# Kernel optimization log

Measured on AMD Instinct MI355X. Metric: run time of the kernel, lower is better.

Reference implementation:

```python
import jax, jax.numpy as jnp
import numpy as np

N = 100000   # number of website nodes
E = 800000   # edges per edge type
F = 128      # in_feats == out_feats
NEG_SLOPE = 0.2


def setup_inputs() -> dict:
    key = jax.random.key(0)
    ks = jax.random.split(key, 16)
    s = 1.0 / np.sqrt(F)
    return {
        "feat": jax.random.normal(ks[0], (N, F), jnp.float32),
        "src_u": jax.random.randint(ks[1], (E,), 0, N),
        "dst_u": jax.random.randint(ks[2], (E,), 0, N),
        "src_r": jax.random.randint(ks[3], (E,), 0, N),
        "dst_r": jax.random.randint(ks[4], (E,), 0, N),
        # fc_self (no bias)
        "W_self": jax.random.uniform(ks[5], (F, F), jnp.float32, -s, s),
        # attn branch 'user'
        "W_u": jax.random.uniform(ks[6], (F, F), jnp.float32, -s, s),
        "a_l_u": jax.random.uniform(ks[7], (F,), jnp.float32, -s, s),
        "a_r_u": jax.random.uniform(ks[8], (F,), jnp.float32, -s, s),
        # attn branch 'reuse'
        "W_r": jax.random.uniform(ks[9], (F, F), jnp.float32, -s, s),
        "a_l_r": jax.random.uniform(ks[10], (F,), jnp.float32, -s, s),
        "a_r_r": jax.random.uniform(ks[11], (F,), jnp.float32, -s, s),
        # fc_neigh (with bias)
        "W_neigh": jax.random.uniform(ks[12], (F, F), jnp.float32, -s, s),
        "b_neigh": jax.random.uniform(ks[13], (F,), jnp.float32, -s, s),
        # module-level bias parameter
        "bias": jnp.zeros((F,), jnp.float32),
    }


def _attn_aggregate(feat, W, a_l, a_r, src, dst, n_nodes):
    """GAT-style single-head aggregation over one edge type.
    Returns [n_nodes, F] = sum_{e: dst(e)=v} softmax_v(leaky_relu(el[src]+er[dst])) * h[src]."""
    h = feat @ W                                    # [N, F] (feat_src == feat_dst)
    el = h @ a_l                                    # [N]
    er = h @ a_r                                    # [N]
    e = jax.nn.leaky_relu(el[src] + er[dst], NEG_SLOPE)   # [E]
    # edge_softmax: normalize over incoming edges of each dst node
    m = jax.ops.segment_max(e, dst, num_segments=n_nodes)  # [N] (-inf for isolated dst, unused)
    ex = jnp.exp(e - m[dst])                        # [E]
    denom = jax.ops.segment_sum(ex, dst, num_segments=n_nodes)  # [N]
    a = ex / denom[dst]                             # [E]
    msg = h[src] * a[:, None]                       # [E, F]
    return jax.ops.segment_sum(msg, dst, num_segments=n_nodes)  # [N, F]


def reference(feat, src_u, dst_u, src_r, dst_r, W_self, W_u, a_l_u, a_r_u,
              W_r, a_l_r, a_r_r, W_neigh, b_neigh, bias):
    n = feat.shape[0]
    neigh_u = _attn_aggregate(feat, W_u, a_l_u, a_r_u, src_u, dst_u, n)
    neigh_r = _attn_aggregate(feat, W_r, a_l_r, a_r_r, src_r, dst_r, n)
    # multi_update_all cross reducer 'mean' over the two edge types
    neigh = 0.5 * (neigh_u + neigh_r)
    h_neigh = neigh @ W_neigh + b_neigh             # fc_neigh
    rst = feat @ W_self + h_neigh                   # fc_self(h_self) + h_neigh
    return rst + bias
```

## Files before the change

### kernel.cpp

```cpp
#include <hip/hip_runtime.h>

#define F 128
#define NEG_SLOPE 0.2f
#define SHIFT 9
#define BPB 512
#define NBS 512

typedef _Float16 f16_t;
typedef _Float16 f16x8 __attribute__((ext_vector_type(8)));
typedef _Float16 f16x2 __attribute__((ext_vector_type(2)));
typedef float f32x4 __attribute__((ext_vector_type(4)));

__global__ __launch_bounds__(128) void prep_mats(
    const float* __restrict__ Wu, const float* __restrict__ Wr,
    const float* __restrict__ Ws, const float* __restrict__ Wn,
    const float* __restrict__ alu, const float* __restrict__ aru,
    const float* __restrict__ alr, const float* __restrict__ arr_,
    f16_t* __restrict__ Mtu, f16_t* __restrict__ Mtr, f16_t* __restrict__ Wts,
    float* __restrict__ wlu, float* __restrict__ wru,
    float* __restrict__ wlr, float* __restrict__ wrr)
{
    int b = blockIdx.x;
    int tid = threadIdx.x;
    if (b < 256) {
        int k = b & 127;
        const float* W = (b < 128) ? Wu : Wr;
        f16_t* M = (b < 128) ? Mtu : Mtr;
        float acc = 0.f;
        for (int t = 0; t < F; t++) acc += W[k * F + t] * Wn[t * F + tid];
        M[tid * F + k] = (f16_t)acc;
    } else if (b < 384) {
        int c = b - 256;
        Wts[c * F + tid] = (f16_t)Ws[tid * F + c];
    } else {
        int which = b - 384;
        const float* W = (which < 2) ? Wu : Wr;
        const float* a = (which == 0) ? alu : (which == 1) ? aru : (which == 2) ? alr : arr_;
        float acc = 0.f;
        for (int c = 0; c < F; c++) acc += W[tid * F + c] * a[c];
        float* o = (which == 0) ? wlu : (which == 1) ? wru : (which == 2) ? wlr : wrr;
        o[tid] = acc;
    }
}


__global__ __launch_bounds__(256) void cast_p1a(
    const float* __restrict__ feat,
    const float* __restrict__ wlu, const float* __restrict__ wru,
    const float* __restrict__ wlr, const float* __restrict__ wrr,
    f16_t* __restrict__ featb,
    float* __restrict__ elu, float* __restrict__ eru,
    float* __restrict__ elr, float* __restrict__ err_,
    const int* __restrict__ dst_u, const int* __restrict__ dst_r,
    int* __restrict__ cnt_bb,
    int Eu, int Et, int N, int chunk, int n, int nbk)
{
    int b = blockIdx.x;
    int tid = threadIdx.x;
    if (b < 256) {
        __shared__ int hist[NBS];
        for (int i = tid; i < NBS; i += 256) hist[i] = 0;
        __syncthreads();
        int e0 = b * chunk;
        int e1 = e0 + chunk; if (e1 > Et) e1 = Et;
        int u1 = (e1 < Eu) ? e1 : Eu;
        for (int e = e0 + tid; e < u1; e += 256) {
            int bin = dst_u[e];
            atomicAdd(&hist[bin >> SHIFT], 1);
        }
        int r0 = (e0 > Eu) ? e0 : Eu;
        for (int e = r0 + tid; e < e1; e += 256) {
            int bin = N + dst_r[e - Eu];
            atomicAdd(&hist[bin >> SHIFT], 1);
        }
        __syncthreads();
        for (int i = tid; i < NBS; i += 256) cnt_bb[b * NBS + i] = hist[i];
        return;
    }
    int fid = b - 256;
    int lane = tid & 63;
    int wave = tid >> 6;
    int lo = lane & 15, hi = lane >> 4;
    int base = fid * 64 + wave * 16;
    if (base >= n) return;
    int row = base + lo;
    if (row > n - 1) row = n - 1;
    const float* fp = feat + (size_t)row * F + hi * 8;
    f16_t* fb = featb + (size_t)row * F + hi * 8;
    const float* wsel = (lo == 0) ? wlu : (lo == 1) ? wru : (lo == 2) ? wlr : wrr;

    f32x4 acc = (f32x4){0.f, 0.f, 0.f, 0.f};
#pragma unroll
    for (int ks = 0; ks < 4; ks++) {
        float4 a0 = *(const float4*)(fp + ks * 32);
        float4 a1 = *(const float4*)(fp + ks * 32 + 4);
        f16x8 af;
        af[0] = (f16_t)a0.x; af[1] = (f16_t)a0.y; af[2] = (f16_t)a0.z; af[3] = (f16_t)a0.w;
        af[4] = (f16_t)a1.x; af[5] = (f16_t)a1.y; af[6] = (f16_t)a1.z; af[7] = (f16_t)a1.w;
        *(f16x8*)(fb + ks * 32) = af;
        f16x8 bf;
#pragma unroll
        for (int q = 0; q < 8; q++) bf[q] = (f16_t)0;
        if (lo < 4) {
            float4 b0 = *(const float4*)(wsel + ks * 32 + hi * 8);
            float4 b1 = *(const float4*)(wsel + ks * 32 + hi * 8 + 4);
            bf[0] = (f16_t)b0.x; bf[1] = (f16_t)b0.y; bf[2] = (f16_t)b0.z; bf[3] = (f16_t)b0.w;
            bf[4] = (f16_t)b1.x; bf[5] = (f16_t)b1.y; bf[6] = (f16_t)b1.z; bf[7] = (f16_t)b1.w;
        }
        acc = __builtin_amdgcn_mfma_f32_16x16x32_f16(af, bf, acc, 0, 0, 0);
    }
    if (lo < 4) {
        float* oarr = (lo == 0) ? elu : (lo == 1) ? eru : (lo == 2) ? elr : err_;
#pragma unroll
        for (int j = 0; j < 4; j++) {
            int r = base + hi * 4 + j;
            if (r < n) oarr[r] = acc[j];
        }
    }
}


__global__ __launch_bounds__(256) void scan_bb1(int* __restrict__ cnt_bb,
                                                int* __restrict__ btot, int nbk)
{
    int k = blockIdx.x;
    int tid = threadIdx.x;
    __shared__ int lds[256];
    int v = cnt_bb[tid * NBS + k];
    lds[tid] = v;
    __syncthreads();
    for (int off = 1; off < 256; off <<= 1) {
        int add = (tid >= off) ? lds[tid - off] : 0;
        __syncthreads();
        lds[tid] += add;
        __syncthreads();
    }
    cnt_bb[tid * NBS + k] = lds[tid] - v;
    if (tid == 255) btot[k] = lds[255];
}


__global__ __launch_bounds__(512) void scan_bb2(const int* __restrict__ btot,
                                                int* __restrict__ bbase,
                                                int* __restrict__ rp,
                                                int nbk, int twoN, int Et)
{
    __shared__ int lds[512];
    int t = threadIdx.x;
    int v = (t < nbk) ? btot[t] : 0;
    lds[t] = v;
    __syncthreads();
    for (int off = 1; off < 512; off <<= 1) {
        int add = (t >= off) ? lds[t - off] : 0;
        __syncthreads();
        lds[t] += add;
        __syncthreads();
    }
    bbase[t] = lds[t] - v;
    if (t == 0) rp[twoN] = Et;
}


__global__ __launch_bounds__(256) void p1b_scatter(
    const int* __restrict__ src_u, const int* __restrict__ dst_u,
    const int* __restrict__ src_r, const int* __restrict__ dst_r,
    const int* __restrict__ cnt_bb, const int* __restrict__ bbase,
    uint2* __restrict__ bucketed,
    int Eu, int Et, int N, int chunk, int nbk)
{
    int b = blockIdx.x;
    int tid = threadIdx.x;
    __shared__ int cur[NBS];
    for (int i = tid; i < nbk; i += 256) cur[i] = bbase[i] + cnt_bb[b * NBS + i];
    __syncthreads();
    int e0 = b * chunk;
    int e1 = e0 + chunk; if (e1 > Et) e1 = Et;
    int u1 = (e1 < Eu) ? e1 : Eu;
    for (int e = e0 + tid; e < u1; e += 256) {
        int bin = dst_u[e];
        int s = src_u[e];
        int pos = atomicAdd(&cur[bin >> SHIFT], 1);
        bucketed[pos] = make_uint2((unsigned)s, (unsigned)bin);
    }
    int r0 = (e0 > Eu) ? e0 : Eu;
    for (int e = r0 + tid; e < e1; e += 256) {
        int bin = N + dst_r[e - Eu];
        int s = src_r[e - Eu];
        int pos = atomicAdd(&cur[bin >> SHIFT], 1);
        bucketed[pos] = make_uint2((unsigned)s, (unsigned)bin);
    }
}


__global__ __launch_bounds__(256) void p2_build(
    const uint2* __restrict__ bucketed, const int* __restrict__ bbase,
    int* __restrict__ rp, int* __restrict__ csr, int twoN)
{
    int k = blockIdx.x;
    int tid = threadIdx.x;
    int beg = bbase[k], end = bbase[k + 1];
    __shared__ int hist[BPB];
    __shared__ int psum[256];
    for (int i = tid; i < BPB; i += 256) hist[i] = 0;
    __syncthreads();
    for (int i = beg + tid; i < end; i += 256) {
        uint2 p = bucketed[i];
        atomicAdd(&hist[p.y & (BPB - 1)], 1);
    }
    __syncthreads();
    int a0 = hist[2 * tid], a1 = hist[2 * tid + 1];
    psum[tid] = a0 + a1;
    __syncthreads();
    for (int off = 1; off < 256; off <<= 1) {
        int add = (tid >= off) ? psum[tid - off] : 0;
        __syncthreads();
        psum[tid] += add;
        __syncthreads();
    }
    int base0 = beg + psum[tid] - (a0 + a1);
    int bin0 = (k << SHIFT) + 2 * tid;
    if (bin0 < twoN)     rp[bin0]     = base0;
    if (bin0 + 1 < twoN) rp[bin0 + 1] = base0 + a0;
    __syncthreads();
    hist[2 * tid]     = base0;
    hist[2 * tid + 1] = base0 + a0;
    __syncthreads();
    for (int i = beg + tid; i < end; i += 256) {
        uint2 p = bucketed[i];
        int pos = atomicAdd(&hist[p.y & (BPB - 1)], 1);
        csr[pos] = (int)p.x;
    }
}


__global__ __launch_bounds__(256) void aggregate_fused(
    const f16_t* __restrict__ featb,
    const float* __restrict__ elu, const float* __restrict__ eru,
    const float* __restrict__ elr, const float* __restrict__ err_,
    const int* __restrict__ rp, const int* __restrict__ csr,
    f16_t* __restrict__ aggu, f16_t* __restrict__ aggr, int n)
{
    int wid = (int)(((size_t)blockIdx.x * 256 + threadIdx.x) >> 6);
    if (wid >= n) return;
    int lane = threadIdx.x & 63;
    int g = lane >> 4, lo = lane & 15;

    int begu = rp[wid],     endu = rp[wid + 1];
    int begr = rp[n + wid], endr = rp[n + wid + 1];
    float ervu = eru[wid];
    float ervr = err_[wid];

    union UP { f16x2 h; int i; };
    union UV { f16x8 v; f16x2 p[4]; };

    f16x2 z = {(f16_t)0, (f16_t)0};
    f16x2 au0 = z, au1 = z, au2 = z, au3 = z;
    f16x2 ar0 = z, ar1 = z, ar2 = z, ar3 = z;
    float du = 0.f, dr = 0.f;

    int iu = begu + g, ir = begr + g;
    int su = (iu < endu) ? csr[iu] : 0;
    int sr = (ir < endr) ? csr[ir] : 0;

    while (iu < endu || ir < endr) {
        int su2 = (iu + 4 < endu) ? csr[iu + 4] : 0;
        int sr2 = (ir + 4 < endr) ? csr[ir + 4] : 0;
        if (iu < endu) {
            float e = elu[su] + ervu;
            e = fmaxf(e, NEG_SLOPE * e);
            float ex = __expf(e);
            f16_t exh = (f16_t)ex;
            f16x2 exv = {exh, exh};
            UV hc; hc.v = *(const f16x8*)&featb[(size_t)su * F + lo * 8];
            au0 += exv * hc.p[0];
            au1 += exv * hc.p[1];
            au2 += exv * hc.p[2];
            au3 += exv * hc.p[3];
            du += ex;
        }
        if (ir < endr) {
            float e = elr[sr] + ervr;
            e = fmaxf(e, NEG_SLOPE * e);
            float ex = __expf(e);
            f16_t exh = (f16_t)ex;
            f16x2 exv = {exh, exh};
            UV hc; hc.v = *(const f16x8*)&featb[(size_t)sr * F + lo * 8];
            ar0 += exv * hc.p[0];
            ar1 += exv * hc.p[1];
            ar2 += exv * hc.p[2];
            ar3 += exv * hc.p[3];
            dr += ex;
        }
        iu += 4; ir += 4; su = su2; sr = sr2;
    }

#pragma unroll
    for (int off = 16; off < 64; off <<= 1) {
        du += __shfl_xor(du, off);
        dr += __shfl_xor(dr, off);
        UP x;
        x.h = au0; x.i = __shfl_xor(x.i, off); au0 += x.h;
        x.h = au1; x.i = __shfl_xor(x.i, off); au1 += x.h;
        x.h = au2; x.i = __shfl_xor(x.i, off); au2 += x.h;
        x.h = au3; x.i = __shfl_xor(x.i, off); au3 += x.h;
        x.h = ar0; x.i = __shfl_xor(x.i, off); ar0 += x.h;
        x.h = ar1; x.i = __shfl_xor(x.i, off); ar1 += x.h;
        x.h = ar2; x.i = __shfl_xor(x.i, off); ar2 += x.h;
        x.h = ar3; x.i = __shfl_xor(x.i, off); ar3 += x.h;
    }

    if (g == 0) {
        float invu = (du > 0.f) ? 0.5f / du : 0.f;
        float invr = (dr > 0.f) ? 0.5f / dr : 0.f;
        f16_t ihu = (f16_t)invu, ihr = (f16_t)invr;
        f16x2 ivu = {ihu, ihu}, ivr = {ihr, ihr};
        UV ou, orr;
        ou.p[0] = au0 * ivu; ou.p[1] = au1 * ivu; ou.p[2] = au2 * ivu; ou.p[3] = au3 * ivu;
        orr.p[0] = ar0 * ivr; orr.p[1] = ar1 * ivr; orr.p[2] = ar2 * ivr; orr.p[3] = ar3 * ivr;
        *(f16x8*)&aggu[(size_t)wid * F + lo * 8] = ou.v;
        *(f16x8*)&aggr[(size_t)wid * F + lo * 8] = orr.v;
    }
}


__global__ __launch_bounds__(1024) void mfma_final3(
    const f16_t* __restrict__ featb,
    const f16_t* __restrict__ aggu, const f16_t* __restrict__ aggr,
    const f16_t* __restrict__ Wts, const f16_t* __restrict__ Mtu,
    const f16_t* __restrict__ Mtr,
    const float* __restrict__ bn, const float* __restrict__ bias,
    float* __restrict__ out, int n, int ntiles)
{
    __shared__ f16_t Ls[F * F];
    __shared__ f16_t Lu[F * F];
    __shared__ f16_t Lr[F * F];
    for (int i = threadIdx.x; i < 2048; i += 1024) {
        int c = i >> 4, kc = i & 15, kcs = kc ^ (c & 15);
        *(f16x8*)&Ls[c * F + kcs * 8] = *(const f16x8*)&Wts[c * F + kc * 8];
        *(f16x8*)&Lu[c * F + kcs * 8] = *(const f16x8*)&Mtu[c * F + kc * 8];
        *(f16x8*)&Lr[c * F + kcs * 8] = *(const f16x8*)&Mtr[c * F + kc * 8];
    }
    __syncthreads();

    int lane = threadIdx.x & 63;
    int wave = threadIdx.x >> 6;
    int lo = lane & 15, hi = lane >> 4;

    float cb[8];
#pragma unroll
    for (int t = 0; t < 8; t++) cb[t] = bn[t * 16 + lo] + bias[t * 16 + lo];

    for (int tile = blockIdx.x; tile < ntiles; tile += 256) {
        int row0 = tile * 256 + wave * 16;
        if (row0 >= n) continue;
        int arow = row0 + lo;
        if (arow > n - 1) arow = n - 1;
        const f16_t* pf = featb + (size_t)arow * F + hi * 8;
        const f16_t* pu = aggu + (size_t)arow * F + hi * 8;
        const f16_t* pr = aggr + (size_t)arow * F + hi * 8;

        f32x4 acc[8];
#pragma unroll
        for (int t = 0; t < 8; t++) acc[t] = (f32x4){0.f, 0.f, 0.f, 0.f};

#pragma unroll
        for (int ks = 0; ks < 4; ks++) {
            f16x8 a1 = *(const f16x8*)(pf + ks * 32);
            f16x8 a2 = *(const f16x8*)(pu + ks * 32);
            f16x8 a3 = *(const f16x8*)(pr + ks * 32);
#pragma unroll
            for (int t = 0; t < 8; t++) {
                int c = t * 16 + lo;
                int kcs = (ks * 4 + hi) ^ lo;
                f16x8 bs = *(const f16x8*)&Ls[c * F + kcs * 8];
                f16x8 bu = *(const f16x8*)&Lu[c * F + kcs * 8];
                f16x8 br = *(const f16x8*)&Lr[c * F + kcs * 8];
                acc[t] = __builtin_amdgcn_mfma_f32_16x16x32_f16(a1, bs, acc[t], 0, 0, 0);
                acc[t] = __builtin_amdgcn_mfma_f32_16x16x32_f16(a2, bu, acc[t], 0, 0, 0);
                acc[t] = __builtin_amdgcn_mfma_f32_16x16x32_f16(a3, br, acc[t], 0, 0, 0);
            }
        }

#pragma unroll
        for (int j = 0; j < 4; j++) {
            int r = row0 + hi * 4 + j;
            if (r < n) {
                float* op = out + (size_t)r * F + lo;
#pragma unroll
                for (int t = 0; t < 8; t++) op[t * 16] = acc[t][j] + cb[t];
            }
        }
    }
}


extern "C" void kernel_launch(void* const* d_in, const int* in_sizes, int n_in,
                              void* d_out, int out_size, void* d_ws, size_t ws_size,
                              hipStream_t stream) {
    const float* feat   = (const float*)d_in[0];
    const int*   src_u  = (const int*)d_in[1];
    const int*   dst_u  = (const int*)d_in[2];
    const int*   src_r  = (const int*)d_in[3];
    const int*   dst_r  = (const int*)d_in[4];
    const float* W_self = (const float*)d_in[5];
    const float* W_u    = (const float*)d_in[6];
    const float* a_l_u  = (const float*)d_in[7];
    const float* a_r_u  = (const float*)d_in[8];
    const float* W_r    = (const float*)d_in[9];
    const float* a_l_r  = (const float*)d_in[10];
    const float* a_r_r  = (const float*)d_in[11];
    const float* W_ngh  = (const float*)d_in[12];
    const float* b_ngh  = (const float*)d_in[13];
    const float* bias   = (const float*)d_in[14];
    float* out = (float*)d_out;

    const int N  = in_sizes[0] / F;
    const int Eu = in_sizes[1];
    const int Er = in_sizes[3];
    const int Et = Eu + Er;
    const int twoN = 2 * N;
    const int nbk = (twoN + BPB - 1) >> SHIFT;

    char* ws = (char*)d_ws;
    size_t off = 0;
    auto alloc = [&](size_t bytes) -> void* {
        void* p = ws + off;
        off = (off + bytes + 255) & ~(size_t)255;
        return p;
    };
    f16_t* featb = (f16_t*)alloc((size_t)N * F * 2);
    f16_t* aggu  = (f16_t*)alloc((size_t)N * F * 2);
    f16_t* aggr  = (f16_t*)alloc((size_t)N * F * 2);
    f16_t* Mt_u  = (f16_t*)alloc((size_t)F * F * 2);
    f16_t* Mt_r  = (f16_t*)alloc((size_t)F * F * 2);
    f16_t* Wt_s  = (f16_t*)alloc((size_t)F * F * 2);
    float* wlu = (float*)alloc((size_t)F * 4);
    float* wru = (float*)alloc((size_t)F * 4);
    float* wlr = (float*)alloc((size_t)F * 4);
    float* wrr = (float*)alloc((size_t)F * 4);
    float* elu = (float*)alloc((size_t)N * 4);
    float* eru = (float*)alloc((size_t)N * 4);
    float* elr = (float*)alloc((size_t)N * 4);
    float* err_ = (float*)alloc((size_t)N * 4);
    int* cnt_bb = (int*)alloc((size_t)256 * NBS * 4);
    int* btot   = (int*)alloc((size_t)NBS * 4);
    int* bbase  = (int*)alloc((size_t)(NBS + 1) * 4);
    int* rp2    = (int*)alloc(((size_t)twoN + 1) * 4);
    uint2* bucketed = (uint2*)alloc((size_t)Et * 8);
    int* csr2   = (int*)alloc((size_t)Et * 4);

    prep_mats<<<388, 128, 0, stream>>>(W_u, W_r, W_self, W_ngh,
                                       a_l_u, a_r_u, a_l_r, a_r_r,
                                       Mt_u, Mt_r, Wt_s, wlu, wru, wlr, wrr);

    const int chunk = (Et + 255) / 256;
    int castBlocks = (N + 63) / 64;
    cast_p1a<<<256 + castBlocks, 256, 0, stream>>>(
        feat, wlu, wru, wlr, wrr, featb, elu, eru, elr, err_,
        dst_u, dst_r, cnt_bb, Eu, Et, N, chunk, N, nbk);

    scan_bb1<<<nbk, 256, 0, stream>>>(cnt_bb, btot, nbk);
    scan_bb2<<<1, 512, 0, stream>>>(btot, bbase, rp2, nbk, twoN, Et);
    p1b_scatter<<<256, 256, 0, stream>>>(src_u, dst_u, src_r, dst_r,
                                         cnt_bb, bbase, bucketed,
                                         Eu, Et, N, chunk, nbk);
    p2_build<<<nbk, 256, 0, stream>>>(bucketed, bbase, rp2, csr2, twoN);

    aggregate_fused<<<(N + 3) / 4, 256, 0, stream>>>(featb, elu, eru, elr, err_,
                                                     rp2, csr2, aggu, aggr, N);
    int ntiles = (N + 255) / 256;
    mfma_final3<<<256, 1024, 0, stream>>>(featb, aggu, aggr,
                                          Wt_s, Mt_u, Mt_r,
                                          b_ngh, bias, out, N, ntiles);
}
```

Before: 156.3 us.

## Precompute edge weights during CSR build and map 16-lane groups per destination

Packs each bucketed edge into one 32-bit word (17-bit source plus the bin's low bits), halving the bucket buffer traffic. The CSR build now also computes the leaky-relu exp attention weight per edge and stores it as fp16 next to the CSR, so aggregation no longer gathers el/er. The aggregation kernel gives each 16-lane group its own destination node instead of a whole wave, which removes the cross-group shuffle reduction, and it double-buffers two edges per type. This adds an fp16 edge-weight array and depends on node ids fitting in 17 bits. It also gives less parallelism per high-degree node.

```diff
diff --git a/kernel.cpp b/kernel.cpp
--- a/kernel.cpp
+++ b/kernel.cpp
@@ -139,7 +139,6 @@
     if (tid == 255) btot[k] = lds[255];
 }
 
-
 __global__ __launch_bounds__(512) void scan_bb2(const int* __restrict__ btot,
                                                 int* __restrict__ bbase,
                                                 int* __restrict__ rp,
@@ -165,7 +164,7 @@
     const int* __restrict__ src_u, const int* __restrict__ dst_u,
     const int* __restrict__ src_r, const int* __restrict__ dst_r,
     const int* __restrict__ cnt_bb, const int* __restrict__ bbase,
-    uint2* __restrict__ bucketed,
+    unsigned* __restrict__ bucketed,
     int Eu, int Et, int N, int chunk, int nbk)
 {
     int b = blockIdx.x;
@@ -180,21 +179,24 @@
         int bin = dst_u[e];
         int s = src_u[e];
         int pos = atomicAdd(&cur[bin >> SHIFT], 1);
-        bucketed[pos] = make_uint2((unsigned)s, (unsigned)bin);
+        bucketed[pos] = (unsigned)s | ((unsigned)(bin & (BPB - 1)) << 17);
     }
     int r0 = (e0 > Eu) ? e0 : Eu;
     for (int e = r0 + tid; e < e1; e += 256) {
         int bin = N + dst_r[e - Eu];
         int s = src_r[e - Eu];
         int pos = atomicAdd(&cur[bin >> SHIFT], 1);
-        bucketed[pos] = make_uint2((unsigned)s, (unsigned)bin);
+        bucketed[pos] = (unsigned)s | ((unsigned)(bin & (BPB - 1)) << 17);
     }
 }
 
 
 __global__ __launch_bounds__(256) void p2_build(
-    const uint2* __restrict__ bucketed, const int* __restrict__ bbase,
-    int* __restrict__ rp, int* __restrict__ csr, int twoN)
+    const unsigned* __restrict__ bucketed, const int* __restrict__ bbase,
+    const float* __restrict__ elu, const float* __restrict__ eru,
+    const float* __restrict__ elr, const float* __restrict__ err_,
+    int* __restrict__ rp, int* __restrict__ csr, f16_t* __restrict__ exh,
+    int twoN, int N)
 {
     int k = blockIdx.x;
     int tid = threadIdx.x;
@@ -204,8 +206,8 @@
     for (int i = tid; i < BPB; i += 256) hist[i] = 0;
     __syncthreads();
     for (int i = beg + tid; i < end; i += 256) {
-        uint2 p = bucketed[i];
-        atomicAdd(&hist[p.y & (BPB - 1)], 1);
+        unsigned w = bucketed[i];
+        atomicAdd(&hist[(w >> 17) & (BPB - 1)], 1);
     }
     __syncthreads();
     int a0 = hist[2 * tid], a1 = hist[2 * tid + 1];
@@ -226,90 +228,111 @@
     hist[2 * tid + 1] = base0 + a0;
     __syncthreads();
     for (int i = beg + tid; i < end; i += 256) {
-        uint2 p = bucketed[i];
-        int pos = atomicAdd(&hist[p.y & (BPB - 1)], 1);
-        csr[pos] = (int)p.x;
-    }
-}
-
-
-__global__ __launch_bounds__(256) void aggregate_fused(
-    const f16_t* __restrict__ featb,
-    const float* __restrict__ elu, const float* __restrict__ eru,
-    const float* __restrict__ elr, const float* __restrict__ err_,
+        unsigned w = bucketed[i];
+        int src = (int)(w & 0x1FFFF);
+        int binlow = (int)((w >> 17) & (BPB - 1));
+        int bin = (k << SHIFT) | binlow;
+        bool isu = bin < N;
+        const float* el = isu ? elu : elr;
+        const float* er = isu ? eru : err_;
+        int d = isu ? bin : bin - N;
+        float e = el[src] + er[d];
+        e = fmaxf(e, NEG_SLOPE * e);
+        float ex = __expf(e);
+        int pos = atomicAdd(&hist[binlow], 1);
+        csr[pos] = src;
+        exh[pos] = (f16_t)ex;
+    }
+}
+
+
+__global__ __launch_bounds__(256) void aggregate_v2(
+    const f16_t* __restrict__ featb, const f16_t* __restrict__ exh,
     const int* __restrict__ rp, const int* __restrict__ csr,
     f16_t* __restrict__ aggu, f16_t* __restrict__ aggr, int n)
 {
-    int wid = (int)(((size_t)blockIdx.x * 256 + threadIdx.x) >> 6);
-    if (wid >= n) return;
+    int wave = (int)(((size_t)blockIdx.x * 256 + threadIdx.x) >> 6);
     int lane = threadIdx.x & 63;
     int g = lane >> 4, lo = lane & 15;
-
-    int begu = rp[wid],     endu = rp[wid + 1];
-    int begr = rp[n + wid], endr = rp[n + wid + 1];
-    float ervu = eru[wid];
-    float ervr = err_[wid];
-
-    union UP { f16x2 h; int i; };
+    int dst = wave * 4 + g;
+    bool alive = (dst < n);
+    int dc = alive ? dst : (n - 1);
+
+    int begu = rp[dc], endu = rp[dc + 1];
+    int begr = rp[n + dc], endr = rp[n + dc + 1];
+    if (!alive) { endu = begu; endr = begr; }
+
     union UV { f16x8 v; f16x2 p[4]; };
-
     f16x2 z = {(f16_t)0, (f16_t)0};
     f16x2 au0 = z, au1 = z, au2 = z, au3 = z;
     f16x2 ar0 = z, ar1 = z, ar2 = z, ar3 = z;
     float du = 0.f, dr = 0.f;
 
-    int iu = begu + g, ir = begr + g;
-    int su = (iu < endu) ? csr[iu] : 0;
-    int sr = (ir < endr) ? csr[ir] : 0;
+    int iu = begu, ir = begr;
+
+    int a0 = (iu     < endu) ? iu     : 0;
+    int a1 = (iu + 1 < endu) ? iu + 1 : 0;
+    int b0 = (ir     < endr) ? ir     : 0;
+    int b1 = (ir + 1 < endr) ? ir + 1 : 0;
+    int cu0 = csr[a0], cu1 = csr[a1], cr0 = csr[b0], cr1 = csr[b1];
+    f16_t wu0 = (iu     < endu) ? exh[a0] : (f16_t)0;
+    f16_t wu1 = (iu + 1 < endu) ? exh[a1] : (f16_t)0;
+    f16_t wr0 = (ir     < endr) ? exh[b0] : (f16_t)0;
+    f16_t wr1 = (ir + 1 < endr) ? exh[b1] : (f16_t)0;
+    UV hu0, hu1, hr0, hr1;
+    hu0.v = *(const f16x8*)&featb[(size_t)cu0 * F + lo * 8];
+    hu1.v = *(const f16x8*)&featb[(size_t)cu1 * F + lo * 8];
+    hr0.v = *(const f16x8*)&featb[(size_t)cr0 * F + lo * 8];
+    hr1.v = *(const f16x8*)&featb[(size_t)cr1 * F + lo * 8];
 
     while (iu < endu || ir < endr) {
-        int su2 = (iu + 4 < endu) ? csr[iu + 4] : 0;
-        int sr2 = (ir + 4 < endr) ? csr[ir + 4] : 0;
-        if (iu < endu) {
-            float e = elu[su] + ervu;
-            e = fmaxf(e, NEG_SLOPE * e);
-            float ex = __expf(e);
-            f16_t exh = (f16_t)ex;
-            f16x2 exv = {exh, exh};
-            UV hc; hc.v = *(const f16x8*)&featb[(size_t)su * F + lo * 8];
-            au0 += exv * hc.p[0];
-            au1 += exv * hc.p[1];
-            au2 += exv * hc.p[2];
-            au3 += exv * hc.p[3];
-            du += ex;
-        }
-        if (ir < endr) {
-            float e = elr[sr] + ervr;
-            e = fmaxf(e, NEG_SLOPE * e);
-            float ex = __expf(e);
-            f16_t exh = (f16_t)ex;
-            f16x2 exv = {exh, exh};
-            UV hc; hc.v = *(const f16x8*)&featb[(size_t)sr * F + lo * 8];
-            ar0 += exv * hc.p[0];
-            ar1 += exv * hc.p[1];
-            ar2 += exv * hc.p[2];
-            ar3 += exv * hc.p[3];
-            dr += ex;
-        }
-        iu += 4; ir += 4; su = su2; sr = sr2;
-    }
-
-#pragma unroll
-    for (int off = 16; off < 64; off <<= 1) {
-        du += __shfl_xor(du, off);
-        dr += __shfl_xor(dr, off);
-        UP x;
-        x.h = au0; x.i = __shfl_xor(x.i, off); au0 += x.h;
-        x.h = au1; x.i = __shfl_xor(x.i, off); au1 += x.h;
-        x.h = au2; x.i = __shfl_xor(x.i, off); au2 += x.h;
-        x.h = au3; x.i = __shfl_xor(x.i, off); au3 += x.h;
-        x.h = ar0; x.i = __shfl_xor(x.i, off); ar0 += x.h;
-        x.h = ar1; x.i = __shfl_xor(x.i, off); ar1 += x.h;
-        x.h = ar2; x.i = __shfl_xor(x.i, off); ar2 += x.h;
-        x.h = ar3; x.i = __shfl_xor(x.i, off); ar3 += x.h;
-    }
-
-    if (g == 0) {
+        int ju = iu + 2, jr = ir + 2;
+        int na0 = (ju     < endu) ? ju     : 0;
+        int na1 = (ju + 1 < endu) ? ju + 1 : 0;
+        int nb0 = (jr     < endr) ? jr     : 0;
+        int nb1 = (jr + 1 < endr) ? jr + 1 : 0;
+        int ncu0 = csr[na0], ncu1 = csr[na1], ncr0 = csr[nb0], ncr1 = csr[nb1];
+        f16_t nwu0 = (ju     < endu) ? exh[na0] : (f16_t)0;
+        f16_t nwu1 = (ju + 1 < endu) ? exh[na1] : (f16_t)0;
+        f16_t nwr0 = (jr     < endr) ? exh[nb0] : (f16_t)0;
+        f16_t nwr1 = (jr + 1 < endr) ? exh[nb1] : (f16_t)0;
+        UV pu0, pu1, pr0, pr1;
+        pu0.v = *(const f16x8*)&featb[(size_t)ncu0 * F + lo * 8];
+        pu1.v = *(const f16x8*)&featb[(size_t)ncu1 * F + lo * 8];
+        pr0.v = *(const f16x8*)&featb[(size_t)ncr0 * F + lo * 8];
+        pr1.v = *(const f16x8*)&featb[(size_t)ncr1 * F + lo * 8];
+
+        {
+            f16x2 wv = {wu0, wu0};
+            au0 += wv * hu0.p[0]; au1 += wv * hu0.p[1];
+            au2 += wv * hu0.p[2]; au3 += wv * hu0.p[3];
+            du += (float)wu0;
+        }
+        {
+            f16x2 wv = {wu1, wu1};
+            au0 += wv * hu1.p[0]; au1 += wv * hu1.p[1];
+            au2 += wv * hu1.p[2]; au3 += wv * hu1.p[3];
+            du += (float)wu1;
+        }
+        {
+            f16x2 wv = {wr0, wr0};
+            ar0 += wv * hr0.p[0]; ar1 += wv * hr0.p[1];
+            ar2 += wv * hr0.p[2]; ar3 += wv * hr0.p[3];
+            dr += (float)wr0;
+        }
+        {
+            f16x2 wv = {wr1, wr1};
+            ar0 += wv * hr1.p[0]; ar1 += wv * hr1.p[1];
+            ar2 += wv * hr1.p[2]; ar3 += wv * hr1.p[3];
+            dr += (float)wr1;
+        }
+
+        hu0 = pu0; hu1 = pu1; hr0 = pr0; hr1 = pr1;
+        wu0 = nwu0; wu1 = nwu1; wr0 = nwr0; wr1 = nwr1;
+        iu = ju; ir = jr;
+    }
+
+    if (alive) {
         float invu = (du > 0.f) ? 0.5f / du : 0.f;
         float invr = (dr > 0.f) ? 0.5f / dr : 0.f;
         f16_t ihu = (f16_t)invu, ihr = (f16_t)invr;
@@ -317,8 +340,8 @@
         UV ou, orr;
         ou.p[0] = au0 * ivu; ou.p[1] = au1 * ivu; ou.p[2] = au2 * ivu; ou.p[3] = au3 * ivu;
         orr.p[0] = ar0 * ivr; orr.p[1] = ar1 * ivr; orr.p[2] = ar2 * ivr; orr.p[3] = ar3 * ivr;
-        *(f16x8*)&aggu[(size_t)wid * F + lo * 8] = ou.v;
-        *(f16x8*)&aggr[(size_t)wid * F + lo * 8] = orr.v;
+        *(f16x8*)&aggu[(size_t)dst * F + lo * 8] = ou.v;
+        *(f16x8*)&aggr[(size_t)dst * F + lo * 8] = orr.v;
     }
 }
 
@@ -446,8 +469,9 @@
     int* btot   = (int*)alloc((size_t)NBS * 4);
     int* bbase  = (int*)alloc((size_t)(NBS + 1) * 4);
     int* rp2    = (int*)alloc(((size_t)twoN + 1) * 4);
-    uint2* bucketed = (uint2*)alloc((size_t)Et * 8);
+    unsigned* bucketed = (unsigned*)alloc((size_t)Et * 4);
     int* csr2   = (int*)alloc((size_t)Et * 4);
+    f16_t* exh  = (f16_t*)alloc((size_t)Et * 2);
 
     prep_mats<<<388, 128, 0, stream>>>(W_u, W_r, W_self, W_ngh,
                                        a_l_u, a_r_u, a_l_r, a_r_r,
@@ -464,10 +488,11 @@
     p1b_scatter<<<256, 256, 0, stream>>>(src_u, dst_u, src_r, dst_r,
                                          cnt_bb, bbase, bucketed,
                                          Eu, Et, N, chunk, nbk);
-    p2_build<<<nbk, 256, 0, stream>>>(bucketed, bbase, rp2, csr2, twoN);
-
-    aggregate_fused<<<(N + 3) / 4, 256, 0, stream>>>(featb, elu, eru, elr, err_,
-                                                     rp2, csr2, aggu, aggr, N);
+    p2_build<<<nbk, 256, 0, stream>>>(bucketed, bbase, elu, eru, elr, err_,
+                                      rp2, csr2, exh, twoN, N);
+
+    aggregate_v2<<<(N + 15) / 16, 256, 0, stream>>>(featb, exh, rp2, csr2,
+                                                    aggu, aggr, N);
     int ntiles = (N + 255) / 256;
     mfma_final3<<<256, 1024, 0, stream>>>(featb, aggu, aggr,
                                           Wt_s, Mt_u, Mt_r,
```

After: 158.4 us. No clear change (+1.4%).

## Fuse attention aggregation into MFMA output kernel and pack bucketed edges to 32 bits

Applied to the files above, without the earlier changes.

The gather-aggregate kernel is merged into the MFMA projection kernel. Each lane now accumulates the softmax-weighted neighbour sum for one destination row directly in registers and feeds it to the MFMA as the A operand, so the f16 aggu/aggr intermediate buffers are no longer written and read back. Bucketed edges are packed into one 32-bit word (17-bit source plus 9-bit local bin) instead of a uint2, and p2_build now uses 512 threads with one bin per thread. The trade-off is that each lane walks a whole destination's edge list serially, so load balance is worse and register pressure in the fused kernel rises. The 17-bit packing also assumes N is below 131072.

```diff
diff --git a/kernel.cpp b/kernel.cpp
--- a/kernel.cpp
+++ b/kernel.cpp
@@ -139,7 +139,6 @@
     if (tid == 255) btot[k] = lds[255];
 }
 
-
 __global__ __launch_bounds__(512) void scan_bb2(const int* __restrict__ btot,
                                                 int* __restrict__ bbase,
                                                 int* __restrict__ rp,
@@ -165,7 +164,7 @@
     const int* __restrict__ src_u, const int* __restrict__ dst_u,
     const int* __restrict__ src_r, const int* __restrict__ dst_r,
     const int* __restrict__ cnt_bb, const int* __restrict__ bbase,
-    uint2* __restrict__ bucketed,
+    unsigned* __restrict__ bucketed,
     int Eu, int Et, int N, int chunk, int nbk)
 {
     int b = blockIdx.x;
@@ -180,152 +179,62 @@
         int bin = dst_u[e];
         int s = src_u[e];
         int pos = atomicAdd(&cur[bin >> SHIFT], 1);
-        bucketed[pos] = make_uint2((unsigned)s, (unsigned)bin);
+        bucketed[pos] = (unsigned)s | ((unsigned)(bin & (BPB - 1)) << 17);
     }
     int r0 = (e0 > Eu) ? e0 : Eu;
     for (int e = r0 + tid; e < e1; e += 256) {
         int bin = N + dst_r[e - Eu];
         int s = src_r[e - Eu];
         int pos = atomicAdd(&cur[bin >> SHIFT], 1);
-        bucketed[pos] = make_uint2((unsigned)s, (unsigned)bin);
-    }
-}
-
-
-__global__ __launch_bounds__(256) void p2_build(
-    const uint2* __restrict__ bucketed, const int* __restrict__ bbase,
+        bucketed[pos] = (unsigned)s | ((unsigned)(bin & (BPB - 1)) << 17);
+    }
+}
+
+
+__global__ __launch_bounds__(512) void p2_build(
+    const unsigned* __restrict__ bucketed, const int* __restrict__ bbase,
     int* __restrict__ rp, int* __restrict__ csr, int twoN)
 {
     int k = blockIdx.x;
     int tid = threadIdx.x;
     int beg = bbase[k], end = bbase[k + 1];
     __shared__ int hist[BPB];
-    __shared__ int psum[256];
-    for (int i = tid; i < BPB; i += 256) hist[i] = 0;
-    __syncthreads();
-    for (int i = beg + tid; i < end; i += 256) {
-        uint2 p = bucketed[i];
-        atomicAdd(&hist[p.y & (BPB - 1)], 1);
-    }
-    __syncthreads();
-    int a0 = hist[2 * tid], a1 = hist[2 * tid + 1];
-    psum[tid] = a0 + a1;
-    __syncthreads();
-    for (int off = 1; off < 256; off <<= 1) {
+    __shared__ int psum[512];
+    hist[tid] = 0;
+    __syncthreads();
+    for (int i = beg + tid; i < end; i += 512) {
+        unsigned w = bucketed[i];
+        atomicAdd(&hist[(w >> 17) & (BPB - 1)], 1);
+    }
+    __syncthreads();
+    int v = hist[tid];
+    psum[tid] = v;
+    __syncthreads();
+    for (int off = 1; off < 512; off <<= 1) {
         int add = (tid >= off) ? psum[tid - off] : 0;
         __syncthreads();
         psum[tid] += add;
         __syncthreads();
     }
-    int base0 = beg + psum[tid] - (a0 + a1);
-    int bin0 = (k << SHIFT) + 2 * tid;
-    if (bin0 < twoN)     rp[bin0]     = base0;
-    if (bin0 + 1 < twoN) rp[bin0 + 1] = base0 + a0;
-    __syncthreads();
-    hist[2 * tid]     = base0;
-    hist[2 * tid + 1] = base0 + a0;
-    __syncthreads();
-    for (int i = beg + tid; i < end; i += 256) {
-        uint2 p = bucketed[i];
-        int pos = atomicAdd(&hist[p.y & (BPB - 1)], 1);
-        csr[pos] = (int)p.x;
-    }
-}
-
-
-__global__ __launch_bounds__(256) void aggregate_fused(
+    int base = beg + psum[tid] - v;
+    int bin = (k << SHIFT) + tid;
+    if (bin < twoN) rp[bin] = base;
+    hist[tid] = base;
+    __syncthreads();
+    for (int i = beg + tid; i < end; i += 512) {
+        unsigned w = bucketed[i];
+        int src = (int)(w & 0x1FFFF);
+        int pos = atomicAdd(&hist[(w >> 17) & (BPB - 1)], 1);
+        csr[pos] = src;
+    }
+}
+
+
+__global__ __launch_bounds__(1024) void aggregate_final(
     const f16_t* __restrict__ featb,
     const float* __restrict__ elu, const float* __restrict__ eru,
     const float* __restrict__ elr, const float* __restrict__ err_,
     const int* __restrict__ rp, const int* __restrict__ csr,
-    f16_t* __restrict__ aggu, f16_t* __restrict__ aggr, int n)
-{
-    int wid = (int)(((size_t)blockIdx.x * 256 + threadIdx.x) >> 6);
-    if (wid >= n) return;
-    int lane = threadIdx.x & 63;
-    int g = lane >> 4, lo = lane & 15;
-
-    int begu = rp[wid],     endu = rp[wid + 1];
-    int begr = rp[n + wid], endr = rp[n + wid + 1];
-    float ervu = eru[wid];
-    float ervr = err_[wid];
-
-    union UP { f16x2 h; int i; };
-    union UV { f16x8 v; f16x2 p[4]; };
-
-    f16x2 z = {(f16_t)0, (f16_t)0};
-    f16x2 au0 = z, au1 = z, au2 = z, au3 = z;
-    f16x2 ar0 = z, ar1 = z, ar2 = z, ar3 = z;
-    float du = 0.f, dr = 0.f;
-
-    int iu = begu + g, ir = begr + g;
-    int su = (iu < endu) ? csr[iu] : 0;
-    int sr = (ir < endr) ? csr[ir] : 0;
-
-    while (iu < endu || ir < endr) {
-        int su2 = (iu + 4 < endu) ? csr[iu + 4] : 0;
-        int sr2 = (ir + 4 < endr) ? csr[ir + 4] : 0;
-        if (iu < endu) {
-            float e = elu[su] + ervu;
-            e = fmaxf(e, NEG_SLOPE * e);
-            float ex = __expf(e);
-            f16_t exh = (f16_t)ex;
-            f16x2 exv = {exh, exh};
-            UV hc; hc.v = *(const f16x8*)&featb[(size_t)su * F + lo * 8];
-            au0 += exv * hc.p[0];
-            au1 += exv * hc.p[1];
-            au2 += exv * hc.p[2];
-            au3 += exv * hc.p[3];
-            du += ex;
-        }
-        if (ir < endr) {
-            float e = elr[sr] + ervr;
-            e = fmaxf(e, NEG_SLOPE * e);
-            float ex = __expf(e);
-            f16_t exh = (f16_t)ex;
-            f16x2 exv = {exh, exh};
-            UV hc; hc.v = *(const f16x8*)&featb[(size_t)sr * F + lo * 8];
-            ar0 += exv * hc.p[0];
-            ar1 += exv * hc.p[1];
-            ar2 += exv * hc.p[2];
-            ar3 += exv * hc.p[3];
-            dr += ex;
-        }
-        iu += 4; ir += 4; su = su2; sr = sr2;
-    }
-
-#pragma unroll
-    for (int off = 16; off < 64; off <<= 1) {
-        du += __shfl_xor(du, off);
-        dr += __shfl_xor(dr, off);
-        UP x;
-        x.h = au0; x.i = __shfl_xor(x.i, off); au0 += x.h;
-        x.h = au1; x.i = __shfl_xor(x.i, off); au1 += x.h;
-        x.h = au2; x.i = __shfl_xor(x.i, off); au2 += x.h;
-        x.h = au3; x.i = __shfl_xor(x.i, off); au3 += x.h;
-        x.h = ar0; x.i = __shfl_xor(x.i, off); ar0 += x.h;
-        x.h = ar1; x.i = __shfl_xor(x.i, off); ar1 += x.h;
-        x.h = ar2; x.i = __shfl_xor(x.i, off); ar2 += x.h;
-        x.h = ar3; x.i = __shfl_xor(x.i, off); ar3 += x.h;
-    }
-
-    if (g == 0) {
-        float invu = (du > 0.f) ? 0.5f / du : 0.f;
-        float invr = (dr > 0.f) ? 0.5f / dr : 0.f;
-        f16_t ihu = (f16_t)invu, ihr = (f16_t)invr;
-        f16x2 ivu = {ihu, ihu}, ivr = {ihr, ihr};
-        UV ou, orr;
-        ou.p[0] = au0 * ivu; ou.p[1] = au1 * ivu; ou.p[2] = au2 * ivu; ou.p[3] = au3 * ivu;
-        orr.p[0] = ar0 * ivr; orr.p[1] = ar1 * ivr; orr.p[2] = ar2 * ivr; orr.p[3] = ar3 * ivr;
-        *(f16x8*)&aggu[(size_t)wid * F + lo * 8] = ou.v;
-        *(f16x8*)&aggr[(size_t)wid * F + lo * 8] = orr.v;
-    }
-}
-
-
-__global__ __launch_bounds__(1024) void mfma_final3(
-    const f16_t* __restrict__ featb,
-    const f16_t* __restrict__ aggu, const f16_t* __restrict__ aggr,
     const f16_t* __restrict__ Wts, const f16_t* __restrict__ Mtu,
     const f16_t* __restrict__ Mtr,
     const float* __restrict__ bn, const float* __restrict__ bias,
@@ -343,22 +252,83 @@
     __syncthreads();
 
     int lane = threadIdx.x & 63;
-    int wave = threadIdx.x >> 6;
+    int wavIn = threadIdx.x >> 6;
     int lo = lane & 15, hi = lane >> 4;
+    int gwave = blockIdx.x * 16 + wavIn;
+    int nwaves = gridDim.x * 16;
 
     float cb[8];
 #pragma unroll
     for (int t = 0; t < 8; t++) cb[t] = bn[t * 16 + lo] + bias[t * 16 + lo];
 
-    for (int tile = blockIdx.x; tile < ntiles; tile += 256) {
-        int row0 = tile * 256 + wave * 16;
-        if (row0 >= n) continue;
-        int arow = row0 + lo;
-        if (arow > n - 1) arow = n - 1;
-        const f16_t* pf = featb + (size_t)arow * F + hi * 8;
-        const f16_t* pu = aggu + (size_t)arow * F + hi * 8;
-        const f16_t* pr = aggr + (size_t)arow * F + hi * 8;
-
+    for (int tile = gwave; tile < ntiles; tile += nwaves) {
+        int row0 = tile * 16;
+        int dst = row0 + lo;
+        if (dst > n - 1) dst = n - 1;
+        int iu = rp[dst], endu = rp[dst + 1];
+        int ir = rp[n + dst], endr = rp[n + dst + 1];
+        float ervu = eru[dst], ervr = err_[dst];
+
+        f16x8 au[4], ar4[4];
+#pragma unroll
+        for (int ks = 0; ks < 4; ks++) {
+#pragma unroll
+            for (int q = 0; q < 8; q++) { au[ks][q] = (f16_t)0; ar4[ks][q] = (f16_t)0; }
+        }
+        float du = 0.f, dr = 0.f;
+
+        bool vu = iu < endu, vr = ir < endr;
+        int su = vu ? csr[iu] : 0;
+        int sr = vr ? csr[ir] : 0;
+        while (vu || vr) {
+            bool vu2 = (iu + 1) < endu, vr2 = (ir + 1) < endr;
+            int su2 = vu2 ? csr[iu + 1] : 0;
+            int sr2 = vr2 ? csr[ir + 1] : 0;
+            if (vu) {
+                const f16_t* p = featb + (size_t)su * F + hi * 8;
+                f16x8 h0 = *(const f16x8*)(p);
+                f16x8 h1 = *(const f16x8*)(p + 32);
+                f16x8 h2 = *(const f16x8*)(p + 64);
+                f16x8 h3 = *(const f16x8*)(p + 96);
+                float e = elu[su] + ervu;
+                e = fmaxf(e, NEG_SLOPE * e);
+                float ex = __expf(e);
+                f16_t w = (f16_t)ex;
+                f16x8 wv;
+#pragma unroll
+                for (int q = 0; q < 8; q++) wv[q] = w;
+                au[0] += wv * h0; au[1] += wv * h1;
+                au[2] += wv * h2; au[3] += wv * h3;
+                du += ex;
+            }
+            if (vr) {
+                const f16_t* p = featb + (size_t)sr * F + hi * 8;
+                f16x8 h0 = *(const f16x8*)(p);
+                f16x8 h1 = *(const f16x8*)(p + 32);
+                f16x8 h2 = *(const f16x8*)(p + 64);
+                f16x8 h3 = *(const f16x8*)(p + 96);
+                float e = elr[sr] + ervr;
+                e = fmaxf(e, NEG_SLOPE * e);
+                float ex = __expf(e);
+                f16_t w = (f16_t)ex;
+                f16x8 wv;
+#pragma unroll
+                for (int q = 0; q < 8; q++) wv[q] = w;
+                ar4[0] += wv * h0; ar4[1] += wv * h1;
+                ar4[2] += wv * h2; ar4[3] += wv * h3;
+                dr += ex;
+            }
+            iu++; ir++; su = su2; sr = sr2; vu = vu2; vr = vr2;
+        }
+
+        float invu = (du > 0.f) ? 0.5f / du : 0.f;
+        float invr = (dr > 0.f) ? 0.5f / dr : 0.f;
+        f16_t ihu = (f16_t)invu, ihr = (f16_t)invr;
+        f16x8 svu, svr;
+#pragma unroll
+        for (int q = 0; q < 8; q++) { svu[q] = ihu; svr[q] = ihr; }
+
+        const f16_t* pf = featb + (size_t)dst * F + hi * 8;
         f32x4 acc[8];
 #pragma unroll
         for (int t = 0; t < 8; t++) acc[t] = (f32x4){0.f, 0.f, 0.f, 0.f};
@@ -366,12 +336,12 @@
 #pragma unroll
         for (int ks = 0; ks < 4; ks++) {
             f16x8 a1 = *(const f16x8*)(pf + ks * 32);
-            f16x8 a2 = *(const f16x8*)(pu + ks * 32);
-            f16x8 a3 = *(const f16x8*)(pr + ks * 32);
+            f16x8 a2 = au[ks] * svu;
+            f16x8 a3 = ar4[ks] * svr;
+            int kcs = (ks * 4 + hi) ^ lo;
 #pragma unroll
             for (int t = 0; t < 8; t++) {
                 int c = t * 16 + lo;
-                int kcs = (ks * 4 + hi) ^ lo;
                 f16x8 bs = *(const f16x8*)&Ls[c * F + kcs * 8];
                 f16x8 bu = *(const f16x8*)&Lu[c * F + kcs * 8];
                 f16x8 br = *(const f16x8*)&Lr[c * F + kcs * 8];
@@ -429,8 +399,6 @@
         return p;
     };
     f16_t* featb = (f16_t*)alloc((size_t)N * F * 2);
-    f16_t* aggu  = (f16_t*)alloc((size_t)N * F * 2);
-    f16_t* aggr  = (f16_t*)alloc((size_t)N * F * 2);
     f16_t* Mt_u  = (f16_t*)alloc((size_t)F * F * 2);
     f16_t* Mt_r  = (f16_t*)alloc((size_t)F * F * 2);
     f16_t* Wt_s  = (f16_t*)alloc((size_t)F * F * 2);
@@ -446,7 +414,7 @@
     int* btot   = (int*)alloc((size_t)NBS * 4);
     int* bbase  = (int*)alloc((size_t)(NBS + 1) * 4);
     int* rp2    = (int*)alloc(((size_t)twoN + 1) * 4);
-    uint2* bucketed = (uint2*)alloc((size_t)Et * 8);
+    unsigned* bucketed = (unsigned*)alloc((size_t)Et * 4);
     int* csr2   = (int*)alloc((size_t)Et * 4);
 
     prep_mats<<<388, 128, 0, stream>>>(W_u, W_r, W_self, W_ngh,
@@ -464,12 +432,10 @@
     p1b_scatter<<<256, 256, 0, stream>>>(src_u, dst_u, src_r, dst_r,
                                          cnt_bb, bbase, bucketed,
                                          Eu, Et, N, chunk, nbk);
-    p2_build<<<nbk, 256, 0, stream>>>(bucketed, bbase, rp2, csr2, twoN);
-
-    aggregate_fused<<<(N + 3) / 4, 256, 0, stream>>>(featb, elu, eru, elr, err_,
-                                                     rp2, csr2, aggu, aggr, N);
-    int ntiles = (N + 255) / 256;
-    mfma_final3<<<256, 1024, 0, stream>>>(featb, aggu, aggr,
-                                          Wt_s, Mt_u, Mt_r,
-                                          b_ngh, bias, out, N, ntiles);
-}
+    p2_build<<<nbk, 512, 0, stream>>>(bucketed, bbase, rp2, csr2, twoN);
+
+    int ntiles = (N + 15) / 16;
+    aggregate_final<<<256, 1024, 0, stream>>>(featb, elu, eru, elr, err_,
+                                              rp2, csr2, Wt_s, Mt_u, Mt_r,
+                                              b_ngh, bias, out, N, ntiles);
+}
```

Measured after the change: 384.9 us. +146.3%, slower.
